# Performance work log

Hardware: AMD Instinct MI355X
Metric: run time of the kernel (lower is better)

The kernel has to match this reference:

```python
import jax, jax.numpy as jnp
import numpy as np

E, H, L = 512, 1024, 4
VS, VT = 32000, 32000
B, SS, TT = 64, 48, 48
PAD = 0


def _cell(x, h, c, Wih, Whh, bih, bhh):
    # torch.nn.LSTMCell math: gate order i, f, g, o
    g = x @ Wih.T + h @ Whh.T + bih + bhh
    i, f, gg, o = jnp.split(g, 4, axis=-1)
    c = jax.nn.sigmoid(f) * c + jax.nn.sigmoid(i) * jnp.tanh(gg)
    h = jax.nn.sigmoid(o) * jnp.tanh(c)
    return h, c


def setup_inputs() -> dict:
    key = jax.random.key(0)
    ks = jax.random.split(key, 14)
    s = 0.05
    d = {}
    d['src_tokens'] = jax.random.randint(ks[0], (SS, B), 0, VS, dtype=jnp.int32)
    d['tgt_tokens'] = jax.random.randint(ks[1], (TT, B), 0, VT, dtype=jnp.int32)
    d['src_emb'] = jax.random.normal(ks[2], (VS, E)) * s
    d['tgt_emb'] = jax.random.normal(ks[3], (VT, E)) * s
    d['enc_Wih0'] = jax.random.normal(ks[4], (4 * H, E)) * s
    d['enc_WihR'] = jax.random.normal(ks[5], (L - 1, 4 * H, H)) * s
    d['enc_Whh'] = jax.random.normal(ks[6], (L, 4 * H, H)) * s
    d['enc_bih'] = jnp.zeros((L, 4 * H))
    d['enc_bhh'] = jnp.zeros((L, 4 * H))
    d['dec_Wih0'] = jax.random.normal(ks[7], (4 * H, E + H)) * s
    d['dec_WihR'] = jax.random.normal(ks[8], (L - 1, 4 * H, H)) * s
    d['dec_Whh'] = jax.random.normal(ks[9], (L, 4 * H, H)) * s
    d['dec_bih'] = jnp.zeros((L, 4 * H))
    d['dec_bhh'] = jnp.zeros((L, 4 * H))
    d['att_vec_W'] = jax.random.normal(ks[10], (H, 2 * H)) * s
    d['readout_W'] = jax.random.normal(ks[11], (VT, H)) * s
    return d


def _forward(src_tokens, tgt_tokens, src_emb, tgt_emb, enc_Wih0, enc_WihR,
             enc_Whh, enc_bih, enc_bhh, dec_Wih0, dec_WihR, dec_Whh, dec_bih,
             dec_bhh, att_vec_W, readout_W):
    src_x = src_emb[src_tokens]                      # [SS, B, E]
    h0 = jnp.zeros((L, B, H), src_emb.dtype)
    c0 = jnp.zeros((L, B, H), src_emb.dtype)

    def enc_step(carry, x_t):
        h, c = carry
        inp = x_t
        hs, cs = [], []
        for l in range(L):
            Wih = enc_Wih0 if l == 0 else enc_WihR[l - 1]
            hn, cn = _cell(inp, h[l], c[l], Wih, enc_Whh[l], enc_bih[l], enc_bhh[l])
            hs.append(hn); cs.append(cn)
            inp = hn
        return (jnp.stack(hs), jnp.stack(cs)), inp

    (hT, cT), enc_out = jax.lax.scan(enc_step, (h0, c0), src_x)
    src_enc = enc_out.transpose(1, 0, 2)             # [B, SS, H]

    # decoder init: last encoder layer (h, c) copied to every decoder layer
    hd = jnp.tile(hT[-1][None], (L, 1, 1))
    cd = jnp.tile(cT[-1][None], (L, 1, 1))
    tgt_x = tgt_emb[tgt_tokens[:-1]]                 # [TT-1, B, E]
    att0 = jnp.zeros((B, H), src_emb.dtype)

    def dec_step(carry, y_t):
        h, c, att = carry
        inp = jnp.concatenate([y_t, att], axis=-1)   # input feeding
        hs, cs = [], []
        for l in range(L):
            Wih = dec_Wih0 if l == 0 else dec_WihR[l - 1]
            hn, cn = _cell(inp, h[l], c[l], Wih, dec_Whh[l], dec_bih[l], dec_bhh[l])
            hs.append(hn); cs.append(cn)
            inp = hn
        h_top = hs[-1]
        # global attention, 'dot' score (full-length seqs -> all-zero mask is a no-op)
        scores = jnp.einsum('bsh,bh->bs', src_enc, h_top)
        alpha = jax.nn.softmax(scores, axis=-1)
        ctx = jnp.einsum('bs,bsh->bh', alpha, src_enc)
        att_t = jnp.tanh(jnp.concatenate([h_top, ctx], axis=-1) @ att_vec_W.T)
        return (jnp.stack(hs), jnp.stack(cs), att_t), att_t

    _, att_ves = jax.lax.scan(dec_step, (hd, cd, att0), tgt_x)  # [TT-1, B, H]

    logp = jax.nn.log_softmax(att_ves @ readout_W.T, axis=-1)   # [TT-1, B, VT]
    gold = tgt_tokens[1:]
    gold_lp = jnp.take_along_axis(logp, gold[..., None], axis=-1)[..., 0]
    mask = (gold != PAD).astype(logp.dtype)
    return (gold_lp * mask).sum(axis=0)              # [B]


def reference(src_tokens, tgt_tokens, src_emb, tgt_emb, enc_Wih0, enc_WihR,
              enc_Whh, enc_bih, enc_bhh, dec_Wih0, dec_WihR, dec_Whh, dec_bih,
              dec_bhh, att_vec_W, readout_W):
    return _forward(src_tokens, tgt_tokens, src_emb, tgt_emb, enc_Wih0,
                    enc_WihR, enc_Whh, enc_bih, enc_bhh, dec_Wih0, dec_WihR,
                    dec_Whh, dec_bih, dec_bhh, att_vec_W, readout_W)
```

## Files before the change

kernel.cpp:

```cpp
#include <hip/hip_runtime.h>


typedef __attribute__((ext_vector_type(8))) short bf16x8;
typedef __attribute__((ext_vector_type(4))) float f32x4;

#define SMEM_G  49152
#define SMEM_A  65536
#define SMEM_R  40960

#define NMT_SYNC_LIGHT()                                   \
  do {                                                     \
    asm volatile("s_waitcnt lgkmcnt(0)" ::: "memory");     \
    __builtin_amdgcn_s_barrier();                          \
    __builtin_amdgcn_sched_barrier(0);                     \
  } while (0)

__device__ __forceinline__ float bf2f(ushort u) {
  union { uint i; float f; } v; v.i = ((uint)u) << 16; return v.f;
}
__device__ __forceinline__ ushort f2bf(float x) {
  union { float f; uint i; } v; v.f = x;
  uint r = (v.i + 0x7fffu + ((v.i >> 16) & 1u)) >> 16;
  return (ushort)r;
}
__device__ __forceinline__ uint pack2(float x, float y) {
  return (uint)f2bf(x) | ((uint)f2bf(y) << 16);
}
__device__ __forceinline__ float sigm(float x) {
  return __fdividef(1.f, 1.f + __expf(-x));
}
__device__ __forceinline__ float tanhf_fast(float x) {
  const float e = __expf(2.f * x);
  return 1.f - __fdividef(2.f, e + 1.f);
}

__device__ __forceinline__ void gemm_term(
    const ushort* __restrict__ A, int lda,
    const ushort* __restrict__ W, int ldw,
    int K, int m0, int n0,
    f32x4 acc[4], char* s)
{
  const int tid = threadIdx.x;
  const int lane = tid & 63;
  const int w = tid >> 6;
  const int r0 = tid >> 3;
  const int cge = (tid & 7) << 3;
  const int so0 = r0 * 128 + (((tid & 7) << 4) ^ ((r0 & 7) << 4));
  const ushort* Ar0 = A + (size_t)(m0 + r0) * lda + cge;
  const ushort* Ar1 = A + (size_t)(m0 + r0 + 32) * lda + cge;
  const ushort* Wr0 = W + (size_t)(n0 + r0) * ldw + cge;
  const ushort* Wr1 = W + (size_t)(n0 + r0 + 32) * ldw + cge;
  const int NT = K >> 6;

  uint4 a0s0, a1s0, b0s0, b1s0;
  uint4 a0s1, a1s1, b0s1, b1s1;
  uint4 a0s2, a1s2, b0s2, b1s2;

  a0s0 = *(const uint4*)(Ar0);       a1s0 = *(const uint4*)(Ar1);
  b0s0 = *(const uint4*)(Wr0);       b1s0 = *(const uint4*)(Wr1);
  a0s1 = *(const uint4*)(Ar0 + 64);  a1s1 = *(const uint4*)(Ar1 + 64);
  b0s1 = *(const uint4*)(Wr0 + 64);  b1s1 = *(const uint4*)(Wr1 + 64);
  a0s2 = *(const uint4*)(Ar0 + 128); a1s2 = *(const uint4*)(Ar1 + 128);
  b0s2 = *(const uint4*)(Wr0 + 128); b1s2 = *(const uint4*)(Wr1 + 128);
  {
    char* sl = s;
    *(uint4*)(sl + so0) = a0s0;         *(uint4*)(sl + 4096 + so0) = a1s0;
    *(uint4*)(sl + 8192 + so0) = b0s0;  *(uint4*)(sl + 12288 + so0) = b1s0;
    sl = s + 16384;
    *(uint4*)(sl + so0) = a0s1;         *(uint4*)(sl + 4096 + so0) = a1s1;
    *(uint4*)(sl + 8192 + so0) = b0s1;  *(uint4*)(sl + 12288 + so0) = b1s1;
  }
  if (3 < NT) {
    a0s0 = *(const uint4*)(Ar0 + 192); a1s0 = *(const uint4*)(Ar1 + 192);
    b0s0 = *(const uint4*)(Wr0 + 192); b1s0 = *(const uint4*)(Wr1 + 192);
  }
  if (4 < NT) {
    a0s1 = *(const uint4*)(Ar0 + 256); a1s1 = *(const uint4*)(Ar1 + 256);
    b0s1 = *(const uint4*)(Wr0 + 256); b1s1 = *(const uint4*)(Wr1 + 256);
  }

  const int axor = (lane & 7) << 4;
  const int arow = (w * 16 + (lane & 15)) * 128;
  const int brow = (lane & 15) * 128;
  const int kb0 = (lane >> 4) << 4;

#define NMT_ROUND(KR, CUR, ST)                                                \
  do {                                                                        \
    NMT_SYNC_LIGHT();                                                         \
    if ((KR) + 2 < NT) {                                                      \
      char* sl_ = s + (ST) * 16384;                                           \
      *(uint4*)(sl_ + so0) = a0s##ST;                                         \
      *(uint4*)(sl_ + 4096 + so0) = a1s##ST;                                  \
      *(uint4*)(sl_ + 8192 + so0) = b0s##ST;                                  \
      *(uint4*)(sl_ + 12288 + so0) = b1s##ST;                                 \
      if ((KR) + 5 < NT) {                                                    \
        const int off_ = ((KR) + 5) << 6;                                     \
        a0s##ST = *(const uint4*)(Ar0 + off_);                                \
        a1s##ST = *(const uint4*)(Ar1 + off_);                                \
        b0s##ST = *(const uint4*)(Wr0 + off_);                                \
        b1s##ST = *(const uint4*)(Wr1 + off_);                                \
      }                                                                       \
    }                                                                         \
    char* cur_ = s + (CUR) * 16384;                                           \
    _Pragma("unroll")                                                         \
    for (int ks = 0; ks < 2; ++ks) {                                          \
      const int kb = (ks << 6) + kb0;                                         \
      bf16x8 af = *(const bf16x8*)(cur_ + arow + (kb ^ axor));                \
      _Pragma("unroll")                                                       \
      for (int nf = 0; nf < 4; ++nf) {                                        \
        bf16x8 bfr = *(const bf16x8*)(cur_ + 8192 + nf * 2048 + brow +        \
                                      (kb ^ axor));                           \
        acc[nf] = __builtin_amdgcn_mfma_f32_16x16x32_bf16(af, bfr, acc[nf],   \
                                                          0, 0, 0);           \
      }                                                                       \
    }                                                                         \
  } while (0)

  for (int kb_ = 0; kb_ < NT; kb_ += 3) {
    NMT_ROUND(kb_ + 0, 0, 2);
    if (kb_ + 1 < NT) NMT_ROUND(kb_ + 1, 1, 0);
    if (kb_ + 2 < NT) NMT_ROUND(kb_ + 2, 2, 1);
  }
#undef NMT_ROUND
  __syncthreads();
}

__device__ __forceinline__ void att_loadf(
    const float* H0, const float* H1, const float* C0, const float* C1,
    int kt, float4* fh, float4* fc)
{
#pragma unroll
  for (int q = 0; q < 8; ++q) {
    const int rh = q >> 2, sub = (q >> 1) & 1, vq = q & 1;
    const float* hp_ = rh ? H1 : H0;
    const float* cp_ = rh ? C1 : C0;
    fh[q] = *reinterpret_cast<const float4*>(hp_ + kt + sub * 64 + vq * 4);
    fc[q] = *reinterpret_cast<const float4*>(cp_ + kt + sub * 64 + vq * 4);
  }
}

__device__ __forceinline__ void att_store(
    char* buf, int soX, const float4* fh, const float4* fc)
{
#pragma unroll
  for (int rh = 0; rh < 2; ++rh)
#pragma unroll
    for (int sub = 0; sub < 2; ++sub) {
      const int q0 = rh * 4 + sub * 2;
      const float4 u = fh[q0], v = fc[q0];
      const float4 u2 = fh[q0 + 1], v2 = fc[q0 + 1];
      uint4 o;
      o.x = pack2(tanhf_fast(u.x + v.x), tanhf_fast(u.y + v.y));
      o.y = pack2(tanhf_fast(u.z + v.z), tanhf_fast(u.w + v.w));
      o.z = pack2(tanhf_fast(u2.x + v2.x), tanhf_fast(u2.y + v2.y));
      o.w = pack2(tanhf_fast(u2.z + v2.z), tanhf_fast(u2.w + v2.w));
      *reinterpret_cast<uint4*>(buf + sub * 8192 + rh * 4096 + soX) = o;
    }
}

__device__ __forceinline__ void gemm_att(
    const float* __restrict__ H, const float* __restrict__ C2,
    const ushort* __restrict__ W, int ldw, int n0,
    f32x4 acc[4], char* s)
{
  char* sA0 = s;
  char* sB0 = s + 16384;
  char* sA1 = s + 32768;
  char* sB1 = s + 49152;
  const int tid = threadIdx.x;
  const int lane = tid & 63;
  const int w = tid >> 6;
  const int r0 = tid >> 3;
  const int cge = (tid & 7) << 3;
  const int soX = r0 * 128 + (((tid & 7) << 4) ^ ((r0 & 7) << 4));
  const ushort* Wr0 = W + (size_t)(n0 + r0) * ldw + cge;
  const ushort* Wr1 = W + (size_t)(n0 + r0 + 32) * ldw + cge;
  const float* H0 = H + r0 * 1024 + cge;
  const float* H1 = H + (r0 + 32) * 1024 + cge;
  const float* C0 = C2 + r0 * 1024 + cge;
  const float* C1 = C2 + (r0 + 32) * 1024 + cge;

  float4 fh[8], fc[8];
  uint4 b0, b1, b2, b3;
  att_loadf(H0, H1, C0, C1, 0, fh, fc);
  att_store(sA0, soX, fh, fc);
  b0 = *reinterpret_cast<const uint4*>(Wr0);
  b1 = *reinterpret_cast<const uint4*>(Wr1);
  b2 = *reinterpret_cast<const uint4*>(Wr0 + 64);
  b3 = *reinterpret_cast<const uint4*>(Wr1 + 64);
  *reinterpret_cast<uint4*>(sB0 + soX) = b0;
  *reinterpret_cast<uint4*>(sB0 + 4096 + soX) = b1;
  *reinterpret_cast<uint4*>(sB0 + 8192 + soX) = b2;
  *reinterpret_cast<uint4*>(sB0 + 12288 + soX) = b3;
  att_loadf(H0, H1, C0, C1, 128, fh, fc);
  b0 = *reinterpret_cast<const uint4*>(Wr0 + 128);
  b1 = *reinterpret_cast<const uint4*>(Wr1 + 128);
  b2 = *reinterpret_cast<const uint4*>(Wr0 + 192);
  b3 = *reinterpret_cast<const uint4*>(Wr1 + 192);

  const int axor = (lane & 7) << 4;
  const int arow = (w * 16 + (lane & 15)) * 128;
  const int brow = (lane & 15) * 128;
  const int kb0 = (lane >> 4) << 4;
  for (int kt = 0; kt < 1024; kt += 128) {
    char* cA = (kt & 128) ? sA1 : sA0;
    char* cB = (kt & 128) ? sB1 : sB0;
    char* nA = (kt & 128) ? sA0 : sA1;
    char* nB = (kt & 128) ? sB0 : sB1;
    NMT_SYNC_LIGHT();
    if (kt + 128 < 1024) {
      att_store(nA, soX, fh, fc);
      *reinterpret_cast<uint4*>(nB + soX) = b0;
      *reinterpret_cast<uint4*>(nB + 4096 + soX) = b1;
      *reinterpret_cast<uint4*>(nB + 8192 + soX) = b2;
      *reinterpret_cast<uint4*>(nB + 12288 + soX) = b3;
      if (kt + 256 < 1024) {
        att_loadf(H0, H1, C0, C1, kt + 256, fh, fc);
        b0 = *reinterpret_cast<const uint4*>(Wr0 + kt + 256);
        b1 = *reinterpret_cast<const uint4*>(Wr1 + kt + 256);
        b2 = *reinterpret_cast<const uint4*>(Wr0 + kt + 320);
        b3 = *reinterpret_cast<const uint4*>(Wr1 + kt + 320);
      }
    }
#pragma unroll
    for (int ks = 0; ks < 4; ++ks) {
      const int sb = (ks >> 1) * 8192;
      const int kb = ((ks & 1) << 6) + kb0;
      bf16x8 af = *reinterpret_cast<const bf16x8*>(cA + sb + arow + (kb ^ axor));
#pragma unroll
      for (int nf = 0; nf < 4; ++nf) {
        bf16x8 bfr = *reinterpret_cast<const bf16x8*>(
            cB + sb + nf * 2048 + brow + (kb ^ axor));
        acc[nf] = __builtin_amdgcn_mfma_f32_16x16x32_bf16(af, bfr, acc[nf], 0, 0, 0);
      }
    }
  }
  __syncthreads();
}

__device__ __forceinline__ void store_f32(
    float* __restrict__ out, int ldo, int m0, int n0, f32x4 acc[4])
{
  const int tid = threadIdx.x, lane = tid & 63, w = tid >> 6;
  const int rbase = w * 16 + ((lane >> 4) << 2);
  const int cb = lane & 15;
#pragma unroll
  for (int nf = 0; nf < 4; ++nf)
#pragma unroll
    for (int r = 0; r < 4; ++r)
      out[(size_t)(m0 + rbase + r) * ldo + n0 + nf * 16 + cb] = acc[nf][r];
}

__device__ __forceinline__ void cell_store(
    float* smemF, f32x4 acc[4],
    float* __restrict__ c, ushort* __restrict__ hout,
    ushort* __restrict__ senc_t, int j0)
{
  const int tid = threadIdx.x, lane = tid & 63, w = tid >> 6;
  const int rbase = w * 16 + ((lane >> 4) << 2);
  const int cb = lane & 15;
  __syncthreads();
#pragma unroll
  for (int nf = 0; nf < 4; ++nf)
#pragma unroll
    for (int r = 0; r < 4; ++r)
      smemF[(rbase + r) * 68 + nf * 16 + cb] = acc[nf][r];
  __syncthreads();
#pragma unroll
  for (int i = 0; i < 4; ++i) {
    const int id = tid + i * 256;
    const int b = id >> 4, u = id & 15;
    const float g0 = smemF[b * 68 + u * 4 + 0];
    const float g1 = smemF[b * 68 + u * 4 + 1];
    const float g2 = smemF[b * 68 + u * 4 + 2];
    const float g3 = smemF[b * 68 + u * 4 + 3];
    const int off = b * 1024 + j0 + u;
    const float cold = c[off];
    const float cn = sigm(g1) * cold + sigm(g0) * tanhf_fast(g2);
    const float hv = sigm(g3) * tanhf_fast(cn);
    c[off] = cn;
    const ushort hb = f2bf(hv);
    hout[off] = hb;
    if (senc_t) senc_t[(size_t)b * 49152 + j0 + u] = hb;
  }
}

__global__ __launch_bounds__(256) void nmt_init(
    float* c, ushort* henc, float* hbAll, float* ctxAll)
{
  const int idx = blockIdx.x * 256 + threadIdx.x;
  if (idx < 262144) c[idx] = 0.f;
  if (idx < 65536) {
    hbAll[idx] = 0.f;
    ctxAll[idx] = 0.f;
    henc[idx] = 0;
    henc[(size_t)1 * 49 * 65536 + idx] = 0;
    henc[(size_t)2 * 49 * 65536 + idx] = 0;
    henc[(size_t)3 * 49 * 65536 + idx] = 0;
  }
}

__global__ __launch_bounds__(256) void nmt_convperm(
    const float* __restrict__ in, ushort* __restrict__ out,
    int L, int Kin, int col0, int Kout)
{
  const size_t idx = (size_t)blockIdx.x * 256 + threadIdx.x;
  const size_t total = (size_t)L * 4096 * Kout;
  if (idx >= total) return;
  const int k = (int)(idx % Kout);
  const size_t rem = idx / Kout;
  const int rp = (int)(rem % 4096);
  const int l = (int)(rem / 4096);
  const int j = rp >> 2, g = rp & 3;
  out[idx] = f2bf(in[((size_t)l * 4096 + g * 1024 + j) * Kin + col0 + k]);
}

__global__ __launch_bounds__(256) void nmt_convplain(
    const float* __restrict__ in, ushort* __restrict__ out, size_t n)
{
  const size_t idx = (size_t)blockIdx.x * 256 + threadIdx.x;
  if (idx < n) out[idx] = f2bf(in[idx]);
}

__global__ __launch_bounds__(256) void nmt_bias(
    const float* __restrict__ bih, const float* __restrict__ bhh, float* __restrict__ bc)
{
  const int idx = blockIdx.x * 256 + threadIdx.x;
  if (idx >= 4 * 4096) return;
  const int rp = idx & 4095, l = idx >> 12;
  const int j = rp >> 2, g = rp & 3;
  bc[idx] = bih[l * 4096 + g * 1024 + j] + bhh[l * 4096 + g * 1024 + j];
}

__global__ __launch_bounds__(256) void nmt_gather(
    const int* __restrict__ tok, const float* __restrict__ emb,
    ushort* __restrict__ out, int rows)
{
  const size_t idx = (size_t)blockIdx.x * 256 + threadIdx.x;
  if (idx >= (size_t)rows * 512) return;
  const int k = (int)(idx & 511);
  const int r = (int)(idx >> 9);
  out[idx] = f2bf(emb[(size_t)tok[r] * 512 + k]);
}

__global__ __launch_bounds__(256) void nmt_pre(
    const ushort* __restrict__ A, const ushort* __restrict__ Wp,
    const float* __restrict__ bc0, float* __restrict__ out, int K)
{
  __shared__ __align__(16) char smem[SMEM_G];
  const int m0 = blockIdx.x * 64, n0 = blockIdx.y * 64;
  const int lane = threadIdx.x & 63;
  const int cb = lane & 15;
  f32x4 acc[4];
#pragma unroll
  for (int nf = 0; nf < 4; ++nf) {
    const float bv = bc0[n0 + nf * 16 + cb];
#pragma unroll
    for (int r = 0; r < 4; ++r) acc[nf][r] = bv;
  }
  gemm_term(A, K, Wp, K, K, m0, n0, acc, smem);
  store_f32(out, 4096, m0, n0, acc);
}

__global__ __launch_bounds__(256) void nmt_decinit(
    const ushort* __restrict__ henc, float* c, ushort* h)
{
  const int idx = blockIdx.x * 256 + threadIdx.x;
  if (idx >= 65536) return;
  const ushort hv = henc[((size_t)3 * 49 + 48) * 65536 + idx];
  const float cv = c[3 * 65536 + idx];
  c[idx] = cv; c[65536 + idx] = cv; c[2 * 65536 + idx] = cv;
  h[idx] = hv; h[65536 + idx] = hv; h[2 * 65536 + idx] = hv; h[3 * 65536 + idx] = hv;
}

__global__ __launch_bounds__(256) void nmt_sv(
    const ushort* __restrict__ senc, const ushort* __restrict__ attW,
    ushort* __restrict__ SV)
{
  __shared__ __align__(16) char smem[SMEM_G];
  const int b = blockIdx.x;
  const int n0 = blockIdx.y * 64;
  const int tid = threadIdx.x, lane = tid & 63, w = tid >> 6;
  const int rbase = w * 16 + ((lane >> 4) << 2), cb = lane & 15;
  f32x4 acc[4];
#pragma unroll
  for (int nf = 0; nf < 4; ++nf)
#pragma unroll
    for (int r = 0; r < 4; ++r) acc[nf][r] = 0.f;
  gemm_term(senc + (size_t)b * 49152, 1024, attW + 1024, 2048, 1024, 0, n0,
            acc, smem);
#pragma unroll
  for (int nf = 0; nf < 4; ++nf)
#pragma unroll
    for (int r = 0; r < 4; ++r) {
      const int row = rbase + r;
      if (row < 48)
        SV[(size_t)b * 49152 + row * 1024 + n0 + nf * 16 + cb] = f2bf(acc[nf][r]);
    }
}

__global__ __launch_bounds__(256) void nmt_enc_cell(
    int u, int lo, ushort* __restrict__ henc, ushort* __restrict__ srcenc,
    float* __restrict__ c,
    const ushort* __restrict__ WihR, const ushort* __restrict__ Whh,
    const float* __restrict__ X0, const float* __restrict__ bcE)
{
  __shared__ __align__(16) char smem[SMEM_G];
  const int l = lo + blockIdx.y;
  const int t = u - l;
  const int n0 = blockIdx.x * 64;
  const int tid = threadIdx.x, lane = tid & 63, w = tid >> 6;
  const int rbase = w * 16 + ((lane >> 4) << 2), cb = lane & 15;
  f32x4 acc[4];
  if (l == 0) {
#pragma unroll
    for (int nf = 0; nf < 4; ++nf)
#pragma unroll
      for (int r = 0; r < 4; ++r)
        acc[nf][r] = X0[(size_t)t * 262144 + (size_t)(rbase + r) * 4096 + n0 + nf * 16 + cb];
  } else {
#pragma unroll
    for (int nf = 0; nf < 4; ++nf) {
      const float bv = bcE[l * 4096 + n0 + nf * 16 + cb];
#pragma unroll
      for (int r = 0; r < 4; ++r) acc[nf][r] = bv;
    }
    gemm_term(henc + ((size_t)(l - 1) * 49 + t + 1) * 65536, 1024,
              WihR + (size_t)(l - 1) * 4194304, 1024, 1024, 0, n0, acc, smem);
  }
  gemm_term(henc + ((size_t)l * 49 + t) * 65536, 1024,
            Whh + (size_t)l * 4194304, 1024, 1024, 0, n0, acc, smem);
  cell_store((float*)smem, acc, c + l * 65536,
             henc + ((size_t)l * 49 + t + 1) * 65536,
             (l == 3) ? (srcenc + t * 1024) : (ushort*)nullptr, n0 >> 2);
}

__global__ __launch_bounds__(256) void nmt_dec_stage(
    int l, const ushort* __restrict__ hp, ushort* __restrict__ hn,
    float* __restrict__ c,
    const ushort* __restrict__ Whh, const ushort* __restrict__ WihR,
    const ushort* __restrict__ Wd0a,
    const float* __restrict__ hbprev, const float* __restrict__ ctxprev,
    const float* __restrict__ Y0t, const float* __restrict__ bcD,
    float* __restrict__ pbuf)
{
  __shared__ __align__(16) char smem[SMEM_A];
  const int n0 = blockIdx.x * 64;
  const int tid = threadIdx.x, lane = tid & 63, w = tid >> 6;
  const int rbase = w * 16 + ((lane >> 4) << 2), cb = lane & 15;
  f32x4 acc[4];
  if (blockIdx.y == 0) {
    if (l == 0) {
#pragma unroll
      for (int nf = 0; nf < 4; ++nf)
#pragma unroll
        for (int r = 0; r < 4; ++r) {
          const size_t o = (size_t)(rbase + r) * 4096 + n0 + nf * 16 + cb;
          acc[nf][r] = Y0t[o] + pbuf[o];
        }
      gemm_att(hbprev, ctxprev, Wd0a, 1024, n0, acc, smem);
    } else {
#pragma unroll
      for (int nf = 0; nf < 4; ++nf)
#pragma unroll
        for (int r = 0; r < 4; ++r)
          acc[nf][r] = pbuf[(size_t)l * 262144 + (size_t)(rbase + r) * 4096 + n0 + nf * 16 + cb];
      gemm_term(hn + (l - 1) * 65536, 1024, WihR + (size_t)(l - 1) * 4194304,
                1024, 1024, 0, n0, acc, smem);
    }
    cell_store((float*)smem, acc, c + l * 65536, hn + l * 65536,
               (ushort*)nullptr, n0 >> 2);
  } else {
    const int lp = (l + 1) & 3;
    if (lp == 0) {
#pragma unroll
      for (int nf = 0; nf < 4; ++nf)
#pragma unroll
        for (int r = 0; r < 4; ++r) acc[nf][r] = 0.f;
      gemm_term(hn, 1024, Whh, 1024, 1024, 0, n0, acc, smem);
    } else {
#pragma unroll
      for (int nf = 0; nf < 4; ++nf) {
        const float bv = bcD[lp * 4096 + n0 + nf * 16 + cb];
#pragma unroll
        for (int r = 0; r < 4; ++r) acc[nf][r] = bv;
      }
      gemm_term(hp + lp * 65536, 1024, Whh + (size_t)lp * 4194304,
                1024, 1024, 0, n0, acc, smem);
    }
    store_f32(pbuf + (size_t)lp * 262144, 4096, 0, n0, acc);
  }
}

__global__ __launch_bounds__(256) void nmt_partial0(
    const ushort* __restrict__ h0, const ushort* __restrict__ Whh0,
    float* __restrict__ pbuf)
{
  __shared__ __align__(16) char smem[SMEM_G];
  const int n0 = blockIdx.x * 64;
  f32x4 acc[4];
#pragma unroll
  for (int nf = 0; nf < 4; ++nf)
#pragma unroll
    for (int r = 0; r < 4; ++r) acc[nf][r] = 0.f;
  gemm_term(h0, 1024, Whh0, 1024, 1024, 0, n0, acc, smem);
  store_f32(pbuf, 4096, 0, n0, acc);
}

__global__ __launch_bounds__(256) void nmt_attnAB(
    const ushort* __restrict__ h3, const ushort* __restrict__ senc,
    const ushort* __restrict__ SV, const ushort* __restrict__ attW,
    float* __restrict__ ctx2, float* __restrict__ hb)
{
  __shared__ __align__(16) char smem[SMEM_G];
  const int bid = blockIdx.x;
  const int tid = threadIdx.x, lane = tid & 63, w = tid >> 6;
  if (bid < 64) {
    float* sc = (float*)smem;
    float* al = (float*)smem + 64;
    const int b = bid;
    const ushort* sb = senc + (size_t)b * 49152;
    const ushort* vb = SV + (size_t)b * 49152;
    float hreg[16];
#pragma unroll
    for (int q = 0; q < 16; ++q) hreg[q] = bf2f(h3[b * 1024 + lane * 16 + q]);
    for (int s = w; s < 48; s += 4) {
      const ushort* vr = sb + s * 1024 + lane * 16;
      float p = 0.f;
#pragma unroll
      for (int q = 0; q < 16; ++q) p += bf2f(vr[q]) * hreg[q];
      for (int d = 1; d < 64; d <<= 1) p += __shfl_xor(p, d);
      if (lane == 0) sc[s] = p;
    }
    __syncthreads();
    if (tid < 64) {
      const float v = (lane < 48) ? sc[lane] : -3.4e38f;
      float m = v;
      for (int d = 1; d < 64; d <<= 1) m = fmaxf(m, __shfl_xor(m, d));
      float e = (lane < 48) ? expf(v - m) : 0.f;
      float s = e;
      for (int d = 1; d < 64; d <<= 1) s += __shfl_xor(s, d);
      al[lane] = e / s;
    }
    __syncthreads();
    const int k0 = tid * 4;
    float a0 = 0, a1 = 0, a2 = 0, a3 = 0;
    for (int s = 0; s < 48; ++s) {
      const float als = al[s];
      const ushort* vr = vb + s * 1024 + k0;
      a0 += als * bf2f(vr[0]); a1 += als * bf2f(vr[1]);
      a2 += als * bf2f(vr[2]); a3 += als * bf2f(vr[3]);
    }
    ctx2[b * 1024 + k0 + 0] = a0; ctx2[b * 1024 + k0 + 1] = a1;
    ctx2[b * 1024 + k0 + 2] = a2; ctx2[b * 1024 + k0 + 3] = a3;
  } else {
    const int n0 = (bid - 64) * 64;
    f32x4 acc[4];
#pragma unroll
    for (int nf = 0; nf < 4; ++nf)
#pragma unroll
      for (int r = 0; r < 4; ++r) acc[nf][r] = 0.f;
    gemm_term(h3, 1024, attW, 2048, 1024, 0, n0, acc, smem);
    store_f32(hb, 1024, 0, n0, acc);
  }
}

__global__ __launch_bounds__(256) void nmt_attves_k(
    const float* __restrict__ hbAll, const float* __restrict__ ctxAll,
    ushort* __restrict__ attves)
{
  const int i = blockIdx.x * 1024 + threadIdx.x * 4;
#pragma unroll
  for (int k = 0; k < 4; ++k) {
    const int j = i + k;
    attves[j] = f2bf(tanhf_fast(hbAll[j + 65536] + ctxAll[j + 65536]));
  }
}

__global__ __launch_bounds__(256) void nmt_readout(
    const ushort* __restrict__ attves, const ushort* __restrict__ routW,
    const int* __restrict__ tgt, float* __restrict__ pmax,
    float* __restrict__ psum, float* __restrict__ goldl)
{
  __shared__ __align__(16) char smem[SMEM_R];
  const int g = blockIdx.x;
  const int n0 = blockIdx.y * 64;
  const int tid = threadIdx.x, lane = tid & 63, w = tid >> 6;
  const int rbase = w * 16 + ((lane >> 4) << 2), cb = lane & 15;
  const int r0 = tid >> 3;
  const int cge = (tid & 7) << 3;
  const int soX = r0 * 128 + (((tid & 7) << 4) ^ ((r0 & 7) << 4));
  const int axor = (lane & 7) << 4;
  const int arow = (w * 16 + (lane & 15)) * 128;
  const int brow = (lane & 15) * 128;
  const int kb0 = (lane >> 4) << 4;

  f32x4 acc[4][4];
#pragma unroll
  for (int mi = 0; mi < 4; ++mi)
#pragma unroll
    for (int nf = 0; nf < 4; ++nf)
#pragma unroll
      for (int r = 0; r < 4; ++r) acc[mi][nf][r] = 0.f;

  for (int kt = 0; kt < 1024; kt += 64) {
    __syncthreads();
#pragma unroll
    for (int mi = 0; mi < 4; ++mi) {
      const size_t mr = (size_t)(g * 256 + mi * 64 + r0) * 1024 + kt + cge;
      *(uint4*)(smem + mi * 8192 + soX) = *(const uint4*)(attves + mr);
      *(uint4*)(smem + mi * 8192 + 4096 + soX) = *(const uint4*)(attves + mr + 32 * 1024);
    }
    {
      const size_t wr = (size_t)(n0 + r0) * 1024 + kt + cge;
      *(uint4*)(smem + 32768 + soX) = *(const uint4*)(routW + wr);
      *(uint4*)(smem + 32768 + 4096 + soX) = *(const uint4*)(routW + wr + 32 * 1024);
    }
    __syncthreads();
#pragma unroll
    for (int ks = 0; ks < 2; ++ks) {
      const int kb = (ks << 6) + kb0;
      bf16x8 bf0 = *(const bf16x8*)(smem + 32768 + 0 * 2048 + brow + (kb ^ axor));
      bf16x8 bf1 = *(const bf16x8*)(smem + 32768 + 1 * 2048 + brow + (kb ^ axor));
      bf16x8 bf2 = *(const bf16x8*)(smem + 32768 + 2 * 2048 + brow + (kb ^ axor));
      bf16x8 bf3 = *(const bf16x8*)(smem + 32768 + 3 * 2048 + brow + (kb ^ axor));
#pragma unroll
      for (int mi = 0; mi < 4; ++mi) {
        bf16x8 af = *(const bf16x8*)(smem + mi * 8192 + arow + (kb ^ axor));
        acc[mi][0] = __builtin_amdgcn_mfma_f32_16x16x32_bf16(af, bf0, acc[mi][0], 0, 0, 0);
        acc[mi][1] = __builtin_amdgcn_mfma_f32_16x16x32_bf16(af, bf1, acc[mi][1], 0, 0, 0);
        acc[mi][2] = __builtin_amdgcn_mfma_f32_16x16x32_bf16(af, bf2, acc[mi][2], 0, 0, 0);
        acc[mi][3] = __builtin_amdgcn_mfma_f32_16x16x32_bf16(af, bf3, acc[mi][3], 0, 0, 0);
      }
    }
  }

#pragma unroll
  for (int mi = 0; mi < 4; ++mi) {
    const int gm = g * 4 + mi;
    if (gm >= 47) continue;
#pragma unroll
    for (int r = 0; r < 4; ++r) {
      float lm = fmaxf(fmaxf(acc[mi][0][r], acc[mi][1][r]),
                       fmaxf(acc[mi][2][r], acc[mi][3][r]));
      for (int d = 1; d < 16; d <<= 1) lm = fmaxf(lm, __shfl_xor(lm, d));
      float ls = 0.f;
#pragma unroll
      for (int nf = 0; nf < 4; ++nf) ls += expf(acc[mi][nf][r] - lm);
      for (int d = 1; d < 16; d <<= 1) ls += __shfl_xor(ls, d);
      const int grow = gm * 64 + rbase + r;
      if (cb == 0) {
        pmax[(size_t)grow * 500 + blockIdx.y] = lm;
        psum[(size_t)grow * 500 + blockIdx.y] = ls;
      }
      const int t = grow >> 6, b = grow & 63;
      const int gold = tgt[(t + 1) * 64 + b];
#pragma unroll
      for (int nf = 0; nf < 4; ++nf)
        if (n0 + nf * 16 + cb == gold) goldl[grow] = acc[mi][nf][r];
    }
  }
}

__global__ __launch_bounds__(64) void nmt_combine(
    const float* __restrict__ pmax, const float* __restrict__ psum,
    const float* __restrict__ goldl, const int* __restrict__ tgt,
    float* __restrict__ lpm)
{
  const int row = blockIdx.x;
  const int lane = threadIdx.x;
  float m = -3.4e38f, s = 0.f;
  for (int i = lane; i < 500; i += 64) {
    const float pm = pmax[(size_t)row * 500 + i];
    const float ps = psum[(size_t)row * 500 + i];
    if (pm > m) { s = s * expf(m - pm) + ps; m = pm; }
    else        { s += ps * expf(pm - m); }
  }
  for (int d = 1; d < 64; d <<= 1) {
    const float om = __shfl_xor(m, d), os = __shfl_xor(s, d);
    if (om > m) { s = s * expf(m - om) + os; m = om; }
    else        { s += os * expf(om - m); }
  }
  if (lane == 0) {
    const int t = row >> 6, b = row & 63;
    const int gold = tgt[(t + 1) * 64 + b];
    const float lp = goldl[row] - m - logf(s);
    lpm[row] = (gold != 0) ? lp : 0.f;
  }
}

__global__ __launch_bounds__(64) void nmt_final(
    const float* __restrict__ lpm, float* __restrict__ out)
{
  const int b = threadIdx.x;
  float s = 0.f;
  for (int t = 0; t < 47; ++t) s += lpm[t * 64 + b];
  out[b] = s;
}

extern "C" void kernel_launch(void* const* d_in, const int* in_sizes, int n_in,
                              void* d_out, int out_size, void* d_ws, size_t ws_size,
                              hipStream_t stream)
{
  (void)in_sizes; (void)n_in; (void)out_size; (void)ws_size;
  const int*   src_tok  = (const int*)d_in[0];
  const int*   tgt_tok  = (const int*)d_in[1];
  const float* src_emb  = (const float*)d_in[2];
  const float* tgt_emb  = (const float*)d_in[3];
  const float* eWih0    = (const float*)d_in[4];
  const float* eWihR    = (const float*)d_in[5];
  const float* eWhh     = (const float*)d_in[6];
  const float* ebih     = (const float*)d_in[7];
  const float* ebhh     = (const float*)d_in[8];
  const float* dWih0    = (const float*)d_in[9];
  const float* dWihR    = (const float*)d_in[10];
  const float* dWhh     = (const float*)d_in[11];
  const float* dbih     = (const float*)d_in[12];
  const float* dbhh     = (const float*)d_in[13];
  const float* attW_f   = (const float*)d_in[14];
  const float* routW_f  = (const float*)d_in[15];

  char* p = (char*)d_ws;
  auto alloc = [&](size_t bytes) { void* r = (void*)p; p += (bytes + 255) & ~(size_t)255; return r; };
  ushort* eWih0p = (ushort*)alloc((size_t)4096 * 512 * 2);
  ushort* eWihRp = (ushort*)alloc((size_t)3 * 4096 * 1024 * 2);
  ushort* eWhhp  = (ushort*)alloc((size_t)4 * 4096 * 1024 * 2);
  ushort* dWih0y = (ushort*)alloc((size_t)4096 * 512 * 2);
  ushort* dWih0a = (ushort*)alloc((size_t)4096 * 1024 * 2);
  ushort* dWihRp = (ushort*)alloc((size_t)3 * 4096 * 1024 * 2);
  ushort* dWhhp  = (ushort*)alloc((size_t)4 * 4096 * 1024 * 2);
  ushort* attWb  = (ushort*)alloc((size_t)1024 * 2048 * 2);
  ushort* routWb = (ushort*)alloc((size_t)32000 * 1024 * 2);
  ushort* srcx   = (ushort*)alloc((size_t)3072 * 512 * 2);
  ushort* tgtx   = (ushort*)alloc((size_t)3008 * 512 * 2);
  ushort* henc   = (ushort*)alloc((size_t)4 * 49 * 65536 * 2);
  ushort* hA     = (ushort*)alloc((size_t)4 * 65536 * 2);
  ushort* hB     = (ushort*)alloc((size_t)4 * 65536 * 2);
  ushort* srcenc = (ushort*)alloc((size_t)64 * 49152 * 2);
  ushort* SVbuf  = (ushort*)alloc((size_t)64 * 49152 * 2);
  ushort* attves = (ushort*)alloc((size_t)3072 * 1024 * 2);
  float*  hbAll  = (float*)alloc((size_t)48 * 65536 * 4);
  float*  ctxAll = (float*)alloc((size_t)48 * 65536 * 4);
  float*  pbuf   = (float*)alloc((size_t)4 * 262144 * 4);
  float*  X0     = (float*)alloc((size_t)3072 * 4096 * 4);
  float*  Y0     = (float*)alloc((size_t)3008 * 4096 * 4);
  float*  bcE    = (float*)alloc((size_t)16384 * 4);
  float*  bcD    = (float*)alloc((size_t)16384 * 4);
  float*  cbuf   = (float*)alloc((size_t)4 * 65536 * 4);
  float*  pmaxb  = (float*)alloc((size_t)3008 * 500 * 4);
  float*  psumb  = (float*)alloc((size_t)3008 * 500 * 4);
  float*  goldl  = (float*)alloc((size_t)3008 * 4);
  float*  lpm    = (float*)alloc((size_t)3008 * 4);

  const dim3 B256(256);
  auto g1 = [](size_t n) { return dim3((unsigned)((n + 255) / 256)); };

  nmt_init<<<g1(262144), B256, 0, stream>>>(cbuf, henc, hbAll, ctxAll);

  nmt_convperm<<<g1((size_t)4096 * 512), B256, 0, stream>>>(eWih0, eWih0p, 1, 512, 0, 512);
  nmt_convperm<<<g1((size_t)3 * 4096 * 1024), B256, 0, stream>>>(eWihR, eWihRp, 3, 1024, 0, 1024);
  nmt_convperm<<<g1((size_t)4 * 4096 * 1024), B256, 0, stream>>>(eWhh, eWhhp, 4, 1024, 0, 1024);
  nmt_convperm<<<g1((size_t)4096 * 512), B256, 0, stream>>>(dWih0, dWih0y, 1, 1536, 0, 512);
  nmt_convperm<<<g1((size_t)4096 * 1024), B256, 0, stream>>>(dWih0, dWih0a, 1, 1536, 512, 1024);
  nmt_convperm<<<g1((size_t)3 * 4096 * 1024), B256, 0, stream>>>(dWihR, dWihRp, 3, 1024, 0, 1024);
  nmt_convperm<<<g1((size_t)4 * 4096 * 1024), B256, 0, stream>>>(dWhh, dWhhp, 4, 1024, 0, 1024);
  nmt_convplain<<<g1((size_t)1024 * 2048), B256, 0, stream>>>(attW_f, attWb, (size_t)1024 * 2048);
  nmt_convplain<<<g1((size_t)32000 * 1024), B256, 0, stream>>>(routW_f, routWb, (size_t)32000 * 1024);
  nmt_bias<<<g1(16384), B256, 0, stream>>>(ebih, ebhh, bcE);
  nmt_bias<<<g1(16384), B256, 0, stream>>>(dbih, dbhh, bcD);
  nmt_gather<<<g1((size_t)3072 * 512), B256, 0, stream>>>(src_tok, src_emb, srcx, 3072);
  nmt_gather<<<g1((size_t)3008 * 512), B256, 0, stream>>>(tgt_tok, tgt_emb, tgtx, 3008);

  nmt_pre<<<dim3(48, 64), B256, 0, stream>>>(srcx, eWih0p, bcE, X0, 512);
  nmt_pre<<<dim3(47, 64), B256, 0, stream>>>(tgtx, dWih0y, bcD, Y0, 512);

  for (int u = 0; u < 51; ++u) {
    const int lo = (u > 47) ? (u - 47) : 0;
    const int hi = (u < 3) ? u : 3;
    nmt_enc_cell<<<dim3(64, hi - lo + 1), B256, 0, stream>>>(
        u, lo, henc, srcenc, cbuf, eWihRp, eWhhp, X0, bcE);
  }
  nmt_decinit<<<g1(65536), B256, 0, stream>>>(henc, cbuf, hA);
  nmt_sv<<<dim3(64, 16), B256, 0, stream>>>(srcenc, attWb, SVbuf);
  nmt_partial0<<<dim3(64), B256, 0, stream>>>(hA, dWhhp, pbuf);

  for (int t = 0; t < 47; ++t) {
    ushort* hp = (t & 1) ? hB : hA;
    ushort* hn = (t & 1) ? hA : hB;
    for (int l = 0; l < 4; ++l) {
      nmt_dec_stage<<<dim3(64, 2), B256, 0, stream>>>(
          l, hp, hn, cbuf, dWhhp, dWihRp, dWih0a,
          hbAll + (size_t)t * 65536, ctxAll + (size_t)t * 65536,
          Y0 + (size_t)t * 262144, bcD, pbuf);
    }
    nmt_attnAB<<<dim3(80), B256, 0, stream>>>(
        hn + 3 * 65536, srcenc, SVbuf, attWb,
        ctxAll + (size_t)(t + 1) * 65536, hbAll + (size_t)(t + 1) * 65536);
  }
  nmt_attves_k<<<dim3(3008), B256, 0, stream>>>(hbAll, ctxAll, attves);

  nmt_readout<<<dim3(12, 500), B256, 0, stream>>>(attves, routWb, tgt_tok,
                                                  pmaxb, psumb, goldl);
  nmt_combine<<<dim3(3008), dim3(64), 0, stream>>>(pmaxb, psumb, goldl, tgt_tok, lpm);
  nmt_final<<<dim3(1), dim3(64), 0, stream>>>(lpm, (float*)d_out);
}
```

Before: 4.498 ms.

## Batch decoder recurrent Whh partials with attention into one launch per step

Decoder layer-cell kernels now compute only the input-side GEMM plus the cell update, using 64 blocks each. All four layers' recurrent h@Whh partials for the next step run in a single 336-block launch together with the attention score/context and att_vec GEMM. This replaces the interleaved two-role dec_stage grids and removes the hA/hB double buffer. It trades per-cell parallelism for fewer, larger launches, and the serial cell chain now has only 64 blocks per launch.

Result: no change. 4.546 ms (+1.1%).

```diff
diff --git a/kernel.cpp b/kernel.cpp
--- a/kernel.cpp
+++ b/kernel.cpp
@@ -435,90 +435,75 @@
              (l == 3) ? (srcenc + t * 1024) : (ushort*)nullptr, n0 >> 2);
 }
 
-__global__ __launch_bounds__(256) void nmt_dec_stage(
-    int l, const ushort* __restrict__ hp, ushort* __restrict__ hn,
-    float* __restrict__ c,
-    const ushort* __restrict__ Whh, const ushort* __restrict__ WihR,
-    const ushort* __restrict__ Wd0a,
+__global__ __launch_bounds__(256) void nmt_dec_cell(
+    int l, ushort* __restrict__ hn, float* __restrict__ c,
+    const ushort* __restrict__ WihR, const ushort* __restrict__ Wd0a,
     const float* __restrict__ hbprev, const float* __restrict__ ctxprev,
-    const float* __restrict__ Y0t, const float* __restrict__ bcD,
-    float* __restrict__ pbuf)
+    const float* __restrict__ Y0t, float* __restrict__ pbuf)
 {
   __shared__ __align__(16) char smem[SMEM_A];
   const int n0 = blockIdx.x * 64;
   const int tid = threadIdx.x, lane = tid & 63, w = tid >> 6;
   const int rbase = w * 16 + ((lane >> 4) << 2), cb = lane & 15;
   f32x4 acc[4];
-  if (blockIdx.y == 0) {
-    if (l == 0) {
-#pragma unroll
-      for (int nf = 0; nf < 4; ++nf)
-#pragma unroll
-        for (int r = 0; r < 4; ++r) {
-          const size_t o = (size_t)(rbase + r) * 4096 + n0 + nf * 16 + cb;
-          acc[nf][r] = Y0t[o] + pbuf[o];
-        }
-      gemm_att(hbprev, ctxprev, Wd0a, 1024, n0, acc, smem);
-    } else {
-#pragma unroll
-      for (int nf = 0; nf < 4; ++nf)
-#pragma unroll
-        for (int r = 0; r < 4; ++r)
-          acc[nf][r] = pbuf[(size_t)l * 262144 + (size_t)(rbase + r) * 4096 + n0 + nf * 16 + cb];
-      gemm_term(hn + (l - 1) * 65536, 1024, WihR + (size_t)(l - 1) * 4194304,
-                1024, 1024, 0, n0, acc, smem);
-    }
-    cell_store((float*)smem, acc, c + l * 65536, hn + l * 65536,
-               (ushort*)nullptr, n0 >> 2);
+  if (l == 0) {
+#pragma unroll
+    for (int nf = 0; nf < 4; ++nf)
+#pragma unroll
+      for (int r = 0; r < 4; ++r) {
+        const size_t o = (size_t)(rbase + r) * 4096 + n0 + nf * 16 + cb;
+        acc[nf][r] = Y0t[o] + pbuf[o];
+      }
+    gemm_att(hbprev, ctxprev, Wd0a, 1024, n0, acc, smem);
   } else {
-    const int lp = (l + 1) & 3;
-    if (lp == 0) {
-#pragma unroll
-      for (int nf = 0; nf < 4; ++nf)
-#pragma unroll
-        for (int r = 0; r < 4; ++r) acc[nf][r] = 0.f;
-      gemm_term(hn, 1024, Whh, 1024, 1024, 0, n0, acc, smem);
-    } else {
-#pragma unroll
-      for (int nf = 0; nf < 4; ++nf) {
-        const float bv = bcD[lp * 4096 + n0 + nf * 16 + cb];
-#pragma unroll
-        for (int r = 0; r < 4; ++r) acc[nf][r] = bv;
-      }
-      gemm_term(hp + lp * 65536, 1024, Whh + (size_t)lp * 4194304,
-                1024, 1024, 0, n0, acc, smem);
-    }
-    store_f32(pbuf + (size_t)lp * 262144, 4096, 0, n0, acc);
-  }
-}
-
-__global__ __launch_bounds__(256) void nmt_partial0(
-    const ushort* __restrict__ h0, const ushort* __restrict__ Whh0,
-    float* __restrict__ pbuf)
-{
-  __shared__ __align__(16) char smem[SMEM_G];
-  const int n0 = blockIdx.x * 64;
-  f32x4 acc[4];
-#pragma unroll
-  for (int nf = 0; nf < 4; ++nf)
-#pragma unroll
-    for (int r = 0; r < 4; ++r) acc[nf][r] = 0.f;
-  gemm_term(h0, 1024, Whh0, 1024, 1024, 0, n0, acc, smem);
-  store_f32(pbuf, 4096, 0, n0, acc);
-}
-
-__global__ __launch_bounds__(256) void nmt_attnAB(
-    const ushort* __restrict__ h3, const ushort* __restrict__ senc,
-    const ushort* __restrict__ SV, const ushort* __restrict__ attW,
+#pragma unroll
+    for (int nf = 0; nf < 4; ++nf)
+#pragma unroll
+      for (int r = 0; r < 4; ++r)
+        acc[nf][r] = pbuf[(size_t)l * 262144 + (size_t)(rbase + r) * 4096 + n0 + nf * 16 + cb];
+    gemm_term(hn + (l - 1) * 65536, 1024, WihR + (size_t)(l - 1) * 4194304,
+              1024, 1024, 0, n0, acc, smem);
+  }
+  cell_store((float*)smem, acc, c + l * 65536, hn + l * 65536,
+             (ushort*)nullptr, n0 >> 2);
+}
+
+__global__ __launch_bounds__(256) void nmt_dec_big(
+    const ushort* __restrict__ hcur, const ushort* __restrict__ Whh,
+    const float* __restrict__ bcD, float* __restrict__ pbuf,
+    const ushort* __restrict__ senc, const ushort* __restrict__ SV,
+    const ushort* __restrict__ attW,
     float* __restrict__ ctx2, float* __restrict__ hb)
 {
   __shared__ __align__(16) char smem[SMEM_G];
   const int bid = blockIdx.x;
   const int tid = threadIdx.x, lane = tid & 63, w = tid >> 6;
-  if (bid < 64) {
+  const int cb = lane & 15;
+  if (bid < 256) {
+    const int lp = bid >> 6;
+    const int n0 = (bid & 63) * 64;
+    f32x4 acc[4];
+    if (lp == 0) {
+#pragma unroll
+      for (int nf = 0; nf < 4; ++nf)
+#pragma unroll
+        for (int r = 0; r < 4; ++r) acc[nf][r] = 0.f;
+    } else {
+#pragma unroll
+      for (int nf = 0; nf < 4; ++nf) {
+        const float bv = bcD[lp * 4096 + n0 + nf * 16 + cb];
+#pragma unroll
+        for (int r = 0; r < 4; ++r) acc[nf][r] = bv;
+      }
+    }
+    gemm_term(hcur + lp * 65536, 1024, Whh + (size_t)lp * 4194304,
+              1024, 1024, 0, n0, acc, smem);
+    store_f32(pbuf + (size_t)lp * 262144, 4096, 0, n0, acc);
+  } else if (bid < 320) {
+    const ushort* h3 = hcur + 3 * 65536;
     float* sc = (float*)smem;
     float* al = (float*)smem + 64;
-    const int b = bid;
+    const int b = bid - 256;
     const ushort* sb = senc + (size_t)b * 49152;
     const ushort* vb = SV + (size_t)b * 49152;
     float hreg[16];
@@ -554,7 +539,8 @@
     ctx2[b * 1024 + k0 + 0] = a0; ctx2[b * 1024 + k0 + 1] = a1;
     ctx2[b * 1024 + k0 + 2] = a2; ctx2[b * 1024 + k0 + 3] = a3;
   } else {
-    const int n0 = (bid - 64) * 64;
+    const ushort* h3 = hcur + 3 * 65536;
+    const int n0 = (bid - 320) * 64;
     f32x4 acc[4];
 #pragma unroll
     for (int nf = 0; nf < 4; ++nf)
@@ -735,7 +721,6 @@
   ushort* tgtx   = (ushort*)alloc((size_t)3008 * 512 * 2);
   ushort* henc   = (ushort*)alloc((size_t)4 * 49 * 65536 * 2);
   ushort* hA     = (ushort*)alloc((size_t)4 * 65536 * 2);
-  ushort* hB     = (ushort*)alloc((size_t)4 * 65536 * 2);
   ushort* srcenc = (ushort*)alloc((size_t)64 * 49152 * 2);
   ushort* SVbuf  = (ushort*)alloc((size_t)64 * 49152 * 2);
   ushort* attves = (ushort*)alloc((size_t)3072 * 1024 * 2);
@@ -782,19 +767,18 @@
   }
   nmt_decinit<<<g1(65536), B256, 0, stream>>>(henc, cbuf, hA);
   nmt_sv<<<dim3(64, 16), B256, 0, stream>>>(srcenc, attWb, SVbuf);
-  nmt_partial0<<<dim3(64), B256, 0, stream>>>(hA, dWhhp, pbuf);
+  nmt_dec_big<<<dim3(256), B256, 0, stream>>>(
+      hA, dWhhp, bcD, pbuf, srcenc, SVbuf, attWb, ctxAll, hbAll);
 
   for (int t = 0; t < 47; ++t) {
-    ushort* hp = (t & 1) ? hB : hA;
-    ushort* hn = (t & 1) ? hA : hB;
     for (int l = 0; l < 4; ++l) {
-      nmt_dec_stage<<<dim3(64, 2), B256, 0, stream>>>(
-          l, hp, hn, cbuf, dWhhp, dWihRp, dWih0a,
+      nmt_dec_cell<<<dim3(64), B256, 0, stream>>>(
+          l, hA, cbuf, dWihRp, dWih0a,
           hbAll + (size_t)t * 65536, ctxAll + (size_t)t * 65536,
-          Y0 + (size_t)t * 262144, bcD, pbuf);
-    }
-    nmt_attnAB<<<dim3(80), B256, 0, stream>>>(
-        hn + 3 * 65536, srcenc, SVbuf, attWb,
+          Y0 + (size_t)t * 262144, pbuf);
+    }
+    nmt_dec_big<<<dim3(336), B256, 0, stream>>>(
+        hA, dWhhp, bcD, pbuf, srcenc, SVbuf, attWb,
         ctxAll + (size_t)(t + 1) * 65536, hbAll + (size_t)(t + 1) * 65536);
   }
   nmt_attves_k<<<dim3(3008), B256, 0, stream>>>(hbAll, ctxAll, attves);
```
